# Optimization experiments

Measured on AMD Instinct MI355X. Metric: run time of the kernel, lower is better.

Reference implementation:

```python
import jax, jax.numpy as jnp
import numpy as np

B, S, D = 4, 2048, 1024

def setup_inputs() -> dict:
    key = jax.random.key(0)
    k1, k2, k3, k4 = jax.random.split(key, 4)
    output = jax.random.normal(k1, (B, S, D), dtype=jnp.float32)
    # nn.Linear(dim, dim, bias=False): y = x @ W.T ; store W as [D, D]
    scale = 1.0 / np.sqrt(D)
    w_q = jax.random.uniform(k2, (D, D), dtype=jnp.float32, minval=-scale, maxval=scale)
    w_k = jax.random.uniform(k3, (D, D), dtype=jnp.float32, minval=-scale, maxval=scale)
    w_v = jax.random.uniform(k4, (D, D), dtype=jnp.float32, minval=-scale, maxval=scale)
    return {"output": output, "w_q": w_q, "w_k": w_k, "w_v": w_v}

def reference(output, w_q, w_k, w_v):
    # projections: x @ W.T (torch Linear convention)
    q = jnp.einsum('bsd,ed->bse', output, w_q)
    k = jnp.einsum('bsd,ed->bse', output, w_k)
    v = jnp.einsum('bsd,ed->bse', output, w_v)
    scores = jnp.einsum('bqd,bkd->bqk', q, k)      # unscaled, no mask
    attn = jax.nn.softmax(scores, axis=-1)
    return jnp.einsum('bqk,bkd->bqd', attn, v)
```

## Files before the change

kernel.cpp:

```cpp
#include <hip/hip_runtime.h>
#include <hip/hip_bf16.h>
#include <stdint.h>


typedef __attribute__((ext_vector_type(8))) _Float16 f16x8;
typedef __attribute__((ext_vector_type(4))) float f32x4;
typedef __attribute__((ext_vector_type(4))) unsigned short u16x4;

__device__ inline unsigned short f2h(float f) {
    union { _Float16 h; unsigned short u; } x;
    x.h = (_Float16)f;
    return x.u;
}

__device__ inline void async16(const unsigned short* g, unsigned short* l) {
    __builtin_amdgcn_global_load_lds(
        (__attribute__((address_space(1))) void*)g,
        (__attribute__((address_space(3))) void*)l, 16, 0, 0);
}

template <int MODE, int BN>
__global__ __launch_bounds__(256)
void gemm16(const unsigned short* __restrict__ A,
            const unsigned short* __restrict__ B,
            void* __restrict__ C, void* __restrict__ C2,
            int K, int ldA, int ldB, int ldC,
            long sAz, long sBz, long sCz)
{
    constexpr int NT = BN / 32;
    __shared__ __align__(16) unsigned short smem[128 * 64 + BN * 64];
    unsigned short* As = smem;
    unsigned short* Bs = smem + 128 * 64;

    const int tid  = threadIdx.x;
    const int lane = tid & 63;
    const int wave = tid >> 6;
    const int wr   = wave >> 1, wc = wave & 1;
    const int quad = lane >> 4, lrow = lane & 15;
    const int bm   = blockIdx.x, bn = blockIdx.y, z = blockIdx.z;

    const unsigned short* Az = A + (long)z * sAz;
    const unsigned short* Bz = B + (long)z * sBz;

    const unsigned short* gA[4];
    const unsigned short* gB[4];
#pragma unroll
    for (int i = 0; i < 4; ++i) {
        const int l = tid + 256 * i;
        const int r = l >> 3;
        const int c = (l & 7) ^ (r & 7);
        gA[i] = Az + (long)(bm * 128 + r) * ldA + c * 8;
    }
#pragma unroll
    for (int i = 0; i < NT; ++i) {
        const int l = tid + 256 * i;
        const int r = l >> 3;
        const int c = (l & 7) ^ (r & 7);
        gB[i] = Bz + (long)(bn * BN + r) * ldB + c * 8;
    }

    f32x4 acc[4][4];
#pragma unroll
    for (int i = 0; i < 4; ++i)
#pragma unroll
        for (int j = 0; j < NT; ++j)
            acc[i][j] = f32x4{0.f, 0.f, 0.f, 0.f};

    const int fr = lrow & 7;

    for (int k0 = 0; k0 < K; k0 += 64) {
#pragma unroll
        for (int i = 0; i < 4; ++i) async16(gA[i], &As[(tid + 256 * i) * 8]);
#pragma unroll
        for (int i = 0; i < NT; ++i) async16(gB[i], &Bs[(tid + 256 * i) * 8]);
#pragma unroll
        for (int i = 0; i < 4; ++i) gA[i] += 64;
#pragma unroll
        for (int i = 0; i < NT; ++i) gB[i] += 64;
        __syncthreads();

#pragma unroll
        for (int ks = 0; ks < 2; ++ks) {
            const int pc = (((ks << 2) + quad) ^ fr) * 8;
            f16x8 af[4], bf[4];
#pragma unroll
            for (int mt = 0; mt < 4; ++mt)
                af[mt] = *(const f16x8*)&As[(wr * 64 + mt * 16 + lrow) * 64 + pc];
#pragma unroll
            for (int nt = 0; nt < NT; ++nt)
                bf[nt] = *(const f16x8*)&Bs[(wc * (BN / 2) + nt * 16 + lrow) * 64 + pc];
#pragma unroll
            for (int mt = 0; mt < 4; ++mt)
#pragma unroll
                for (int nt = 0; nt < NT; ++nt)
                    acc[mt][nt] = __builtin_amdgcn_mfma_f32_16x16x32_f16(
                        af[mt], bf[nt], acc[mt][nt], 0, 0, 0);
        }
        __syncthreads();
    }

    const int col_base = bn * BN + wc * (BN / 2);

    if (MODE == 1 || (MODE == 0 && z < 2)) {
        const int row_base = bm * 128 + wr * 64;
        const long zC = (long)z * sCz;
#pragma unroll
        for (int mt = 0; mt < 4; ++mt)
#pragma unroll
            for (int nt = 0; nt < NT; ++nt)
#pragma unroll
                for (int r = 0; r < 4; ++r) {
                    const int row = row_base + mt * 16 + quad * 4 + r;
                    const int col = col_base + nt * 16 + lrow;
                    if (MODE == 1)
                        ((float*)C)[zC + (long)row * ldC + col] = acc[mt][nt][r];
                    else
                        ((unsigned short*)C)[zC + (long)row * ldC + col] =
                            f2h(acc[mt][nt][r]);
                }
    } else {
        unsigned short* T = smem;
#pragma unroll
        for (int p = 0; p < 2; ++p) {
            __syncthreads();
            if (wr == p) {
#pragma unroll
                for (int mt = 0; mt < 4; ++mt)
#pragma unroll
                    for (int nt = 0; nt < NT; ++nt) {
                        const int row_l = mt * 16 + quad * 4;
                        const int col_l = wc * (BN / 2) + nt * 16 + lrow;
                        u16x4 pk = {f2h(acc[mt][nt][0]), f2h(acc[mt][nt][1]),
                                    f2h(acc[mt][nt][2]), f2h(acc[mt][nt][3])};
                        *(u16x4*)&T[col_l * 72 + row_l] = pk;
                    }
            }
            __syncthreads();
            const int c  = tid >> 1;
            const int j0 = (tid & 1) * 32;
            const int tok0 = bm * 128 + p * 64;
            const int bb = tok0 >> 11;
            const int s0 = (tok0 & 2047) + j0;
            unsigned short* dst = (unsigned short*)C2 + (long)bb * 2097152 +
                                  (long)(bn * 128 + c) * 2048 + s0;
            const unsigned short* srcT = &T[c * 72 + j0];
#pragma unroll
            for (int i = 0; i < 4; ++i)
                *(f16x8*)(dst + i * 8) = *(const f16x8*)(srcT + i * 8);
        }
    }
}

__global__ __launch_bounds__(256)
void cvt_all(const float* __restrict__ x, const float* __restrict__ w0,
             const float* __restrict__ w1, const float* __restrict__ w2,
             unsigned short* __restrict__ xh, unsigned short* __restrict__ wh)
{
    const int bid = blockIdx.x;
    const float* s;
    unsigned short* d;
    long i;
    if (bid < 4096) {
        s = x; d = xh;
        i = ((long)bid * 256 + threadIdx.x) * 8;
    } else {
        const int wid = bid - 4096;
        const int w = wid >> 9;
        s = (w == 0) ? w0 : (w == 1) ? w1 : w2;
        d = wh + (long)w * 1048576;
        i = ((long)(wid & 511) * 256 + threadIdx.x) * 8;
    }
    f32x4 a = *(const f32x4*)(s + i);
    f32x4 b = *(const f32x4*)(s + i + 4);
    union { unsigned short u[8]; f16x8 v; } t;
#pragma unroll
    for (int j = 0; j < 4; ++j) { t.u[j] = f2h(a[j]); t.u[4 + j] = f2h(b[j]); }
    *(f16x8*)(d + i) = t.v;
}

__global__ __launch_bounds__(256)
void softmax_ip(float* __restrict__ sc)
{
    const long row = blockIdx.x;
    float* srow = sc + row * 2048;
    const int tid = threadIdx.x;

    f32x4 a = *(const f32x4*)(srow + tid * 8);
    f32x4 b = *(const f32x4*)(srow + tid * 8 + 4);
    float v[8];
#pragma unroll
    for (int i = 0; i < 4; ++i) { v[i] = a[i]; v[4 + i] = b[i]; }

    float m = v[0];
#pragma unroll
    for (int i = 1; i < 8; ++i) m = fmaxf(m, v[i]);
#pragma unroll
    for (int off = 32; off; off >>= 1) m = fmaxf(m, __shfl_xor(m, off));

    __shared__ float redm[4], reds[4];
    if ((tid & 63) == 0) redm[tid >> 6] = m;
    __syncthreads();
    m = fmaxf(fmaxf(redm[0], redm[1]), fmaxf(redm[2], redm[3]));

    float s = 0.f;
#pragma unroll
    for (int i = 0; i < 8; ++i) { v[i] = __expf(v[i] - m); s += v[i]; }
#pragma unroll
    for (int off = 32; off; off >>= 1) s += __shfl_xor(s, off);
    if ((tid & 63) == 0) reds[tid >> 6] = s;
    __syncthreads();
    s = reds[0] + reds[1] + reds[2] + reds[3];

    const float inv = 1.f / s;
    union { unsigned short u[8]; f16x8 w; } t;
#pragma unroll
    for (int i = 0; i < 8; ++i) t.u[i] = f2h(v[i] * inv);
    *(f16x8*)((unsigned short*)srow + tid * 8) = t.w;
}

extern "C" void kernel_launch(void* const* d_in, const int* in_sizes, int n_in,
                              void* d_out, int out_size, void* d_ws, size_t ws_size,
                              hipStream_t stream)
{
    const float* x  = (const float*)d_in[0];
    const float* wq = (const float*)d_in[1];
    const float* wk = (const float*)d_in[2];
    const float* wv = (const float*)d_in[3];
    float* out = (float*)d_out;

    char* base = (char*)d_ws;
    const bool batched = (ws_size >= 117440512UL);

    unsigned short* xh = (unsigned short*)base;
    unsigned short* wh = (unsigned short*)(base + 16777216);
    float*          sc = (float*)base;
    unsigned short* q  = (unsigned short*)(base + (batched ? 67108864 : 23068672));
    unsigned short* k  = q + 8388608;
    unsigned short* vt = k + 8388608;

    cvt_all<<<5632, 256, 0, stream>>>(x, wq, wk, wv, xh, wh);

    gemm16<0, 128><<<dim3(64, 8, 3), 256, 0, stream>>>(
        xh, wh, q, vt, 1024, 1024, 1024, 1024, 0L, 1048576L, 8388608L);

    if (batched) {
        gemm16<1, 128><<<dim3(16, 16, 4), 256, 0, stream>>>(
            q, k, sc, nullptr, 1024, 1024, 1024, 2048,
            2097152L, 2097152L, 4194304L);
        softmax_ip<<<8192, 256, 0, stream>>>(sc);
        gemm16<1, 64><<<dim3(16, 16, 4), 256, 0, stream>>>(
            (const unsigned short*)sc, vt, out, nullptr, 2048, 4096, 2048, 1024,
            8388608L, 2097152L, 2097152L);
    } else {
        for (int b = 0; b < 4; ++b) {
            gemm16<1, 128><<<dim3(16, 16, 1), 256, 0, stream>>>(
                q + (long)b * 2097152, k + (long)b * 2097152, sc, nullptr,
                1024, 1024, 1024, 2048, 0L, 0L, 0L);
            softmax_ip<<<2048, 256, 0, stream>>>(sc);
            gemm16<1, 64><<<dim3(16, 16, 1), 256, 0, stream>>>(
                (const unsigned short*)sc, vt + (long)b * 2097152,
                out + (long)b * 2097152, nullptr,
                2048, 4096, 2048, 1024, 0L, 0L, 0L);
        }
    }
}
```

Baseline: 261.8 us.

## Store attention scores in fp16 and enlarge GEMM tiles to 256x512-thread blocks

Scores from QK^T are written as fp16 instead of fp32, and softmax reads and writes them in place as fp16. This halves the traffic for the score matrix in all three stages and shrinks the workspace. All GEMMs now use 512-thread blocks with 256-row tiles, which raises data reuse per block but halves the grid size. The trade-off is fp16 rounding and range risk on the unscaled scores before softmax.

After: 243.9 us. 1.07x faster.

```diff
diff --git a/kernel.cpp b/kernel.cpp
--- a/kernel.cpp
+++ b/kernel.cpp
@@ -12,6 +12,11 @@
     x.h = (_Float16)f;
     return x.u;
 }
+__device__ inline float h2f(unsigned short u) {
+    union { unsigned short u; _Float16 h; } x;
+    x.u = u;
+    return (float)x.h;
+}
 
 __device__ inline void async16(const unsigned short* g, unsigned short* l) {
     __builtin_amdgcn_global_load_lds(
@@ -20,17 +25,18 @@
 }
 
 template <int MODE, int BN>
-__global__ __launch_bounds__(256)
-void gemm16(const unsigned short* __restrict__ A,
-            const unsigned short* __restrict__ B,
-            void* __restrict__ C, void* __restrict__ C2,
-            int K, int ldA, int ldB, int ldC,
-            long sAz, long sBz, long sCz)
+__global__ __launch_bounds__(512)
+void gemm512(const unsigned short* __restrict__ A,
+             const unsigned short* __restrict__ B,
+             void* __restrict__ C, void* __restrict__ C2,
+             int K, int ldA, int ldB, int ldC,
+             long sAz, long sBz, long sCz)
 {
     constexpr int NT = BN / 32;
-    __shared__ __align__(16) unsigned short smem[128 * 64 + BN * 64];
+    constexpr int BI = BN / 64;
+    __shared__ __align__(16) unsigned short smem[256 * 64 + BN * 64];
     unsigned short* As = smem;
-    unsigned short* Bs = smem + 128 * 64;
+    unsigned short* Bs = smem + 256 * 64;
 
     const int tid  = threadIdx.x;
     const int lane = tid & 63;
@@ -43,23 +49,23 @@
     const unsigned short* Bz = B + (long)z * sBz;
 
     const unsigned short* gA[4];
-    const unsigned short* gB[4];
+    const unsigned short* gB[BI];
 #pragma unroll
     for (int i = 0; i < 4; ++i) {
-        const int l = tid + 256 * i;
+        const int l = tid + 512 * i;
         const int r = l >> 3;
         const int c = (l & 7) ^ (r & 7);
-        gA[i] = Az + (long)(bm * 128 + r) * ldA + c * 8;
-    }
-#pragma unroll
-    for (int i = 0; i < NT; ++i) {
-        const int l = tid + 256 * i;
+        gA[i] = Az + (long)(bm * 256 + r) * ldA + c * 8;
+    }
+#pragma unroll
+    for (int i = 0; i < BI; ++i) {
+        const int l = tid + 512 * i;
         const int r = l >> 3;
         const int c = (l & 7) ^ (r & 7);
         gB[i] = Bz + (long)(bn * BN + r) * ldB + c * 8;
     }
 
-    f32x4 acc[4][4];
+    f32x4 acc[4][NT];
 #pragma unroll
     for (int i = 0; i < 4; ++i)
 #pragma unroll
@@ -70,19 +76,19 @@
 
     for (int k0 = 0; k0 < K; k0 += 64) {
 #pragma unroll
-        for (int i = 0; i < 4; ++i) async16(gA[i], &As[(tid + 256 * i) * 8]);
-#pragma unroll
-        for (int i = 0; i < NT; ++i) async16(gB[i], &Bs[(tid + 256 * i) * 8]);
+        for (int i = 0; i < 4; ++i) async16(gA[i], &As[(tid + 512 * i) * 8]);
+#pragma unroll
+        for (int i = 0; i < BI; ++i) async16(gB[i], &Bs[(tid + 512 * i) * 8]);
 #pragma unroll
         for (int i = 0; i < 4; ++i) gA[i] += 64;
 #pragma unroll
-        for (int i = 0; i < NT; ++i) gB[i] += 64;
+        for (int i = 0; i < BI; ++i) gB[i] += 64;
         __syncthreads();
 
 #pragma unroll
         for (int ks = 0; ks < 2; ++ks) {
             const int pc = (((ks << 2) + quad) ^ fr) * 8;
-            f16x8 af[4], bf[4];
+            f16x8 af[4], bf[NT];
 #pragma unroll
             for (int mt = 0; mt < 4; ++mt)
                 af[mt] = *(const f16x8*)&As[(wr * 64 + mt * 16 + lrow) * 64 + pc];
@@ -101,8 +107,8 @@
 
     const int col_base = bn * BN + wc * (BN / 2);
 
-    if (MODE == 1 || (MODE == 0 && z < 2)) {
-        const int row_base = bm * 128 + wr * 64;
+    if (MODE != 0 || z < 2) {
+        const int row_base = bm * 256 + wr * 64;
         const long zC = (long)z * sCz;
 #pragma unroll
         for (int mt = 0; mt < 4; ++mt)
@@ -112,7 +118,7 @@
                 for (int r = 0; r < 4; ++r) {
                     const int row = row_base + mt * 16 + quad * 4 + r;
                     const int col = col_base + nt * 16 + lrow;
-                    if (MODE == 1)
+                    if (MODE == 2)
                         ((float*)C)[zC + (long)row * ldC + col] = acc[mt][nt][r];
                     else
                         ((unsigned short*)C)[zC + (long)row * ldC + col] =
@@ -121,7 +127,7 @@
     } else {
         unsigned short* T = smem;
 #pragma unroll
-        for (int p = 0; p < 2; ++p) {
+        for (int p = 0; p < 4; ++p) {
             __syncthreads();
             if (wr == p) {
 #pragma unroll
@@ -129,24 +135,23 @@
 #pragma unroll
                     for (int nt = 0; nt < NT; ++nt) {
                         const int row_l = mt * 16 + quad * 4;
-                        const int col_l = wc * (BN / 2) + nt * 16 + lrow;
+                        const int col_l = wc * 64 + nt * 16 + lrow;
                         u16x4 pk = {f2h(acc[mt][nt][0]), f2h(acc[mt][nt][1]),
                                     f2h(acc[mt][nt][2]), f2h(acc[mt][nt][3])};
                         *(u16x4*)&T[col_l * 72 + row_l] = pk;
                     }
             }
             __syncthreads();
-            const int c  = tid >> 1;
-            const int j0 = (tid & 1) * 32;
-            const int tok0 = bm * 128 + p * 64;
+            const int c  = tid >> 2;
+            const int j0 = (tid & 3) * 16;
+            const int tok0 = bm * 256 + p * 64;
             const int bb = tok0 >> 11;
             const int s0 = (tok0 & 2047) + j0;
             unsigned short* dst = (unsigned short*)C2 + (long)bb * 2097152 +
                                   (long)(bn * 128 + c) * 2048 + s0;
             const unsigned short* srcT = &T[c * 72 + j0];
-#pragma unroll
-            for (int i = 0; i < 4; ++i)
-                *(f16x8*)(dst + i * 8) = *(const f16x8*)(srcT + i * 8);
+            *(f16x8*)dst = *(const f16x8*)srcT;
+            *(f16x8*)(dst + 8) = *(const f16x8*)(srcT + 8);
         }
     }
 }
@@ -179,17 +184,18 @@
 }
 
 __global__ __launch_bounds__(256)
-void softmax_ip(float* __restrict__ sc)
+void softmax16(unsigned short* __restrict__ sc)
 {
     const long row = blockIdx.x;
-    float* srow = sc + row * 2048;
+    unsigned short* srow = sc + row * 2048;
     const int tid = threadIdx.x;
 
-    f32x4 a = *(const f32x4*)(srow + tid * 8);
-    f32x4 b = *(const f32x4*)(srow + tid * 8 + 4);
+    union { u16x4 p[2]; unsigned short u[8]; } in;
+    in.p[0] = *(const u16x4*)(srow + tid * 8);
+    in.p[1] = *(const u16x4*)(srow + tid * 8 + 4);
     float v[8];
 #pragma unroll
-    for (int i = 0; i < 4; ++i) { v[i] = a[i]; v[4 + i] = b[i]; }
+    for (int i = 0; i < 8; ++i) v[i] = h2f(in.u[i]);
 
     float m = v[0];
 #pragma unroll
@@ -215,7 +221,7 @@
     union { unsigned short u[8]; f16x8 w; } t;
 #pragma unroll
     for (int i = 0; i < 8; ++i) t.u[i] = f2h(v[i] * inv);
-    *(f16x8*)((unsigned short*)srow + tid * 8) = t.w;
+    *(f16x8*)(srow + tid * 8) = t.w;
 }
 
 extern "C" void kernel_launch(void* const* d_in, const int* in_sizes, int n_in,
@@ -229,38 +235,37 @@
     float* out = (float*)d_out;
 
     char* base = (char*)d_ws;
-    const bool batched = (ws_size >= 117440512UL);
+    const bool batched = (ws_size >= 88080384UL);
 
     unsigned short* xh = (unsigned short*)base;
     unsigned short* wh = (unsigned short*)(base + 16777216);
-    float*          sc = (float*)base;
-    unsigned short* q  = (unsigned short*)(base + (batched ? 67108864 : 23068672));
+    unsigned short* sc = (unsigned short*)base;
+    unsigned short* q  = (unsigned short*)(base + (batched ? 33554432 : 23068672));
     unsigned short* k  = q + 8388608;
     unsigned short* vt = k + 8388608;
 
     cvt_all<<<5632, 256, 0, stream>>>(x, wq, wk, wv, xh, wh);
 
-    gemm16<0, 128><<<dim3(64, 8, 3), 256, 0, stream>>>(
+    gemm512<0, 128><<<dim3(32, 8, 3), 512, 0, stream>>>(
         xh, wh, q, vt, 1024, 1024, 1024, 1024, 0L, 1048576L, 8388608L);
 
     if (batched) {
-        gemm16<1, 128><<<dim3(16, 16, 4), 256, 0, stream>>>(
+        gemm512<1, 128><<<dim3(8, 16, 4), 512, 0, stream>>>(
             q, k, sc, nullptr, 1024, 1024, 1024, 2048,
             2097152L, 2097152L, 4194304L);
-        softmax_ip<<<8192, 256, 0, stream>>>(sc);
-        gemm16<1, 64><<<dim3(16, 16, 4), 256, 0, stream>>>(
-            (const unsigned short*)sc, vt, out, nullptr, 2048, 4096, 2048, 1024,
-            8388608L, 2097152L, 2097152L);
+        softmax16<<<8192, 256, 0, stream>>>(sc);
+        gemm512<2, 64><<<dim3(8, 16, 4), 512, 0, stream>>>(
+            sc, vt, out, nullptr, 2048, 2048, 2048, 1024,
+            4194304L, 2097152L, 2097152L);
     } else {
         for (int b = 0; b < 4; ++b) {
-            gemm16<1, 128><<<dim3(16, 16, 1), 256, 0, stream>>>(
+            gemm512<1, 128><<<dim3(8, 16, 1), 512, 0, stream>>>(
                 q + (long)b * 2097152, k + (long)b * 2097152, sc, nullptr,
                 1024, 1024, 1024, 2048, 0L, 0L, 0L);
-            softmax_ip<<<2048, 256, 0, stream>>>(sc);
-            gemm16<1, 64><<<dim3(16, 16, 1), 256, 0, stream>>>(
-                (const unsigned short*)sc, vt + (long)b * 2097152,
-                out + (long)b * 2097152, nullptr,
-                2048, 4096, 2048, 1024, 0L, 0L, 0L);
+            softmax16<<<2048, 256, 0, stream>>>(sc);
+            gemm512<2, 64><<<dim3(8, 16, 1), 512, 0, stream>>>(
+                sc, vt + (long)b * 2097152, out + (long)b * 2097152, nullptr,
+                2048, 2048, 2048, 1024, 0L, 0L, 0L);
         }
     }
 }
```
